# Performance work log

Hardware: AMD Instinct MI355X
Metric: run time of the kernel (lower is better)

The kernel has to match this reference:

```python
import jax, jax.numpy as jnp
import numpy as np
from jax import lax

EPS = 1e-5
DN = ('NCHW', 'OIHW', 'NCHW')


def binarize(x):
    # sign(x) with 0 -> +1, matching _STESign.forward
    return jnp.where(x >= 0, jnp.ones_like(x), -jnp.ones_like(x))


def batchnorm(x, g, b, m, v):
    # inference BatchNorm2d with running stats
    scale = (g / jnp.sqrt(v + EPS))[None, :, None, None]
    shift = (b - m * g / jnp.sqrt(v + EPS))[None, :, None, None]
    return x * scale + shift


def conv(x, w, stride):
    return lax.conv_general_dilated(x, w, (stride, stride), [(1, 1), (1, 1)],
                                    dimension_numbers=DN)


def setup_inputs() -> dict:
    key = jax.random.key(0)
    ks = jax.random.split(key, 24)
    d = {}
    d['x'] = jax.random.normal(ks[0], (32, 3, 224, 224), dtype=jnp.float32)
    d['conv1_w'] = jax.random.normal(ks[1], (32, 3, 3, 3), dtype=jnp.float32) * 0.1
    d['conv2_w'] = jax.random.normal(ks[2], (64, 32, 3, 3), dtype=jnp.float32) * 0.1
    d['conv3_w'] = jax.random.normal(ks[3], (128, 64, 3, 3), dtype=jnp.float32) * 0.1
    d['conv4_w'] = jax.random.normal(ks[4], (256, 128, 3, 3), dtype=jnp.float32) * 0.1
    for i, c in zip(range(1, 5), (32, 64, 128, 256)):
        base = 4 + (i - 1) * 4
        d[f'bn{i}_g'] = jax.random.uniform(ks[base + 1], (c,), dtype=jnp.float32) + 0.5
        d[f'bn{i}_b'] = jax.random.normal(ks[base + 2], (c,), dtype=jnp.float32) * 0.1
        d[f'bn{i}_m'] = jax.random.normal(ks[base + 3], (c,), dtype=jnp.float32) * 0.1
        d[f'bn{i}_v'] = jax.random.uniform(ks[base + 4], (c,), dtype=jnp.float32) + 0.5
    d['fc_w'] = jax.random.normal(ks[21], (2, 256), dtype=jnp.float32) * 0.05
    d['fc_b'] = jnp.zeros((2,), dtype=jnp.float32)
    return d


def reference(x, conv1_w, conv2_w, conv3_w, conv4_w,
              bn1_g, bn1_b, bn1_m, bn1_v,
              bn2_g, bn2_b, bn2_m, bn2_v,
              bn3_g, bn3_b, bn3_m, bn3_v,
              bn4_g, bn4_b, bn4_m, bn4_v,
              fc_w, fc_b):
    # conv1 (real) + bn1
    h = batchnorm(conv(x, conv1_w, 1), bn1_g, bn1_b, bn1_m, bn1_v)
    # BinarizeConv2d: binarize input and weight, then real conv
    h = binarize(batchnorm(conv(binarize(h), binarize(conv2_w), 2), bn2_g, bn2_b, bn2_m, bn2_v))
    h = binarize(batchnorm(conv(binarize(h), binarize(conv3_w), 2), bn3_g, bn3_b, bn3_m, bn3_v))
    h = binarize(batchnorm(conv(binarize(h), binarize(conv4_w), 2), bn4_g, bn4_b, bn4_m, bn4_v))
    # adaptive avg pool to 1x1 -> mean over H,W
    h = jnp.mean(h, axis=(2, 3))  # [B, 256]
    return h @ fc_w.T + fc_b
```

## Files before the change

### kernel.cpp

```cpp
#include <hip/hip_runtime.h>
#include <stdint.h>
#include <math.h>

#define OFF_T2     3712
#define OFF_T3     4224
#define OFF_T4     5248
#define OFF_W2     7296
#define OFF_W3     9600
#define OFF_W4     18816
#define OFF_A1     55680
#define OFF_A2     6478208
#define OFF_A3     9689472
#define OFF_CNT    11295104

#define C2_LW 116
#define C3_LW 58

static __device__ __forceinline__ float2 bnf(float g, float b, float m, float v) {
    float sc = __fdiv_rn(g, __fsqrt_rn(__fadd_rn(v, 1e-5f)));
    float sh = __fsub_rn(b, __fmul_rn(m, sc));
    return make_float2(sc, sh);
}
static __device__ __forceinline__ bool bnpos(float s, float2 p) {
    return __fadd_rn(__fmul_rn(s, p.x), p.y) >= 0.0f;
}
static __device__ __forceinline__ int find_T(int K, float2 p) {
    int lo = -K - 2, hi = K + 2;
    while (lo + 2 < hi) {
        int mid = ((lo + hi) >> 1) & ~1;
        if (bnpos((float)mid, p)) hi = mid; else lo = mid;
    }
    return hi;
}

#define CONV1_BLOCKS 3136
#define PREP_BLOCKS  1586

__global__ __launch_bounds__(256) void k_front(
    const float* __restrict__ x, const float* __restrict__ w1,
    const float* __restrict__ g1, const float* __restrict__ b1,
    const float* __restrict__ m1, const float* __restrict__ v1,
    const float* __restrict__ w2, const float* __restrict__ w3, const float* __restrict__ w4,
    const float* g2, const float* b2, const float* m2, const float* v2,
    const float* g3, const float* b3, const float* m3, const float* v3,
    const float* g4, const float* b4, const float* m4, const float* v4,
    uint32_t* __restrict__ A1,
    int* __restrict__ T2, int* __restrict__ T3, int* __restrict__ T4,
    uint32_t* __restrict__ W2, uint64_t* __restrict__ W3, uint64_t* __restrict__ W4)
{
    int tid = threadIdx.x;
    if (blockIdx.x >= CONV1_BLOCKS) {
        int gtid = (blockIdx.x - CONV1_BLOCKS) * 256 + tid;
        int wid  = gtid >> 6;
        int lane = gtid & 63;
        if (wid < 576) {
            int oc = wid / 9, t = wid - oc * 9;
            float v = (lane < 32) ? w2[oc * 288 + lane * 9 + t] : -1.0f;
            uint64_t m = __ballot(v >= 0.0f);
            if (lane == 0) W2[wid] = (uint32_t)m;
        } else if (wid < 1728) {
            int i = wid - 576;
            int oc = i / 9, t = i - oc * 9;
            float v = w3[oc * 576 + lane * 9 + t];
            uint64_t m = __ballot(v >= 0.0f);
            if (lane == 0) W3[i] = m;
        } else if (wid < 6336) {
            int i = wid - 1728;
            int oc = i / 18, rem = i - oc * 18;
            int t = rem >> 1, h = rem & 1;
            float v = w4[oc * 1152 + (h * 64 + lane) * 9 + t];
            uint64_t m = __ballot(v >= 0.0f);
            if (lane == 0) W4[i] = m;
        } else {
            int c = (wid - 6336) * 64 + lane;
            if (c < 64) {
                T2[c] = find_T(288, bnf(g2[c], b2[c], m2[c], v2[c]));
            } else if (c < 192) {
                int cc = c - 64;
                T3[cc] = find_T(576, bnf(g3[cc], b3[cc], m3[cc], v3[cc]));
            } else if (c < 448) {
                int cc = c - 192;
                T4[cc] = find_T(1152, bnf(g4[cc], b4[cc], m4[cc], v4[cc]));
            }
        }
        return;
    }

    __shared__ float  wl[27 * 32];
    __shared__ float2 s1[32];
    for (int i = tid; i < 864; i += 256) {
        int k = i >> 5, oc = i & 31;
        wl[i] = w1[oc * 27 + k];
    }
    if (tid < 32) s1[tid] = bnf(g1[tid], b1[tid], m1[tid], v1[tid]);
    __syncthreads();

    int idx = blockIdx.x * 256 + tid;
    int xp = idx % 112;
    int t  = idx / 112;
    int y  = t % 224;
    int b  = t / 224;
    int xc = xp * 2;

    const float* xb = x + (size_t)b * 150528;
    float xin[3][3][4];
    if ((unsigned)(y - 1) < 222u && (unsigned)(xp - 1) < 110u) {
        #pragma unroll
        for (int ic = 0; ic < 3; ic++)
            #pragma unroll
            for (int ky = 0; ky < 3; ky++) {
                const float* rp = xb + ic * 50176 + (y - 1 + ky) * 224 + (xc - 1);
                #pragma unroll
                for (int cx = 0; cx < 4; cx++) xin[ic][ky][cx] = rp[cx];
            }
    } else {
        #pragma unroll
        for (int ic = 0; ic < 3; ic++)
            #pragma unroll
            for (int ky = 0; ky < 3; ky++)
                #pragma unroll
                for (int cx = 0; cx < 4; cx++) {
                    int iy = y - 1 + ky, ix = xc - 1 + cx;
                    float v = 0.0f;
                    if ((unsigned)iy < 224u && (unsigned)ix < 224u)
                        v = xb[ic * 50176 + iy * 224 + ix];
                    xin[ic][ky][cx] = v;
                }
    }

    float acc0[32], acc1[32];
    #pragma unroll
    for (int oc = 0; oc < 32; oc++) { acc0[oc] = 0.0f; acc1[oc] = 0.0f; }

    const float4* wl4 = (const float4*)wl;
    #pragma unroll
    for (int k = 0; k < 27; k++) {
        int ic = k / 9, r = (k % 9) / 3, c = k % 3;
        float a0 = xin[ic][r][c];
        float a1 = xin[ic][r][c + 1];
        #pragma unroll
        for (int g8 = 0; g8 < 8; g8++) {
            float4 w = wl4[k * 8 + g8];
            acc0[g8*4+0] = fmaf(a0, w.x, acc0[g8*4+0]);
            acc0[g8*4+1] = fmaf(a0, w.y, acc0[g8*4+1]);
            acc0[g8*4+2] = fmaf(a0, w.z, acc0[g8*4+2]);
            acc0[g8*4+3] = fmaf(a0, w.w, acc0[g8*4+3]);
            acc1[g8*4+0] = fmaf(a1, w.x, acc1[g8*4+0]);
            acc1[g8*4+1] = fmaf(a1, w.y, acc1[g8*4+1]);
            acc1[g8*4+2] = fmaf(a1, w.z, acc1[g8*4+2]);
            acc1[g8*4+3] = fmaf(a1, w.w, acc1[g8*4+3]);
        }
    }

    uint32_t bits0 = 0, bits1 = 0;
    #pragma unroll
    for (int oc = 0; oc < 32; oc++) {
        float2 p = s1[oc];
        bits0 |= (uint32_t)bnpos(acc0[oc], p) << oc;
        bits1 |= (uint32_t)bnpos(acc1[oc], p) << oc;
    }
    uint2* dst = (uint2*)(A1 + (size_t)b * 50176 + y * 224 + xc);
    *dst = make_uint2(bits0, bits1);
}

template<unsigned VM>
static __device__ __forceinline__ bool pred2(const uint32_t (&w)[3][9], int j,
                                             const uint32_t (&wr)[9], int T) {
    int pc = 0;
    #pragma unroll
    for (int ky = 0; ky < 3; ky++)
        #pragma unroll
        for (int kx = 0; kx < 3; kx++) {
            int ti = ky * 3 + kx;
            if (VM & (1u << ti)) pc += __popc(w[ky][2 * j + kx] ^ wr[ti]);
        }
    constexpr int nv = __builtin_popcount(VM);
    return pc <= ((32 * nv - T) >> 1);
}

template<unsigned VM0, unsigned VM>
static __device__ __forceinline__ void group2(const uint32_t* lrow, int g,
        const uint32_t (&wr)[9], int T, uint64_t* dst, int lane) {
    uint32_t win[3][9];
    int c0 = 8 * g;
    #pragma unroll
    for (int r = 0; r < 3; r++) {
        const uint32_t* rp = lrow + r * C2_LW + c0;
        uint4 a = *(const uint4*)(rp);
        uint4 b = *(const uint4*)(rp + 4);
        win[r][0] = a.x; win[r][1] = a.y; win[r][2] = a.z; win[r][3] = a.w;
        win[r][4] = b.x; win[r][5] = b.y; win[r][6] = b.z; win[r][7] = b.w;
        win[r][8] = rp[8];
    }
    uint64_t b0 = __ballot(pred2<VM0>(win, 0, wr, T));
    uint64_t b1 = __ballot(pred2<VM >(win, 1, wr, T));
    uint64_t b2 = __ballot(pred2<VM >(win, 2, wr, T));
    uint64_t b3 = __ballot(pred2<VM >(win, 3, wr, T));
    if (lane == 0) {
        ulonglong2* d = (ulonglong2*)(dst + 4 * g);
        d[0] = make_ulonglong2(b0, b1);
        d[1] = make_ulonglong2(b2, b3);
    }
}

__global__ __launch_bounds__(256) void k_conv2(
    const uint32_t* __restrict__ A1, const uint32_t* __restrict__ W2g,
    const int* __restrict__ T2, uint64_t* __restrict__ A2)
{
    __shared__ __align__(16) uint32_t lds[9 * C2_LW];
    int bi = blockIdx.x;
    int b = bi / 56, rem = bi % 56;
    int oyq = rem >> 1, h = rem & 1;
    int xs = h * 56;
    int tid = threadIdx.x;
    const uint32_t* ap = A1 + (size_t)b * 50176;
    for (int i = tid; i < 9 * C2_LW; i += 256) {
        int r = i / C2_LW, c = i - r * C2_LW;
        int iy = oyq * 8 - 1 + r, ix = 2 * xs - 1 + c;
        uint32_t v = 0;
        if ((unsigned)iy < 224u && (unsigned)ix < 224u) v = ap[iy * 224 + ix];
        lds[i] = v;
    }
    __syncthreads();

    int w = tid >> 6, lane = tid & 63;
    int oy = oyq * 4 + w;
    uint32_t wr[9];
    #pragma unroll
    for (int ti = 0; ti < 9; ti++) wr[ti] = W2g[lane * 9 + ti];
    int T = T2[lane];
    const uint32_t* lrow = lds + 2 * w * C2_LW;
    uint64_t* dst = A2 + (size_t)b * 12544 + oy * 112 + xs;
    bool left = (xs == 0);

    if (oy == 0) {
        if (left) group2<0x1B0, 0x1F8>(lrow, 0, wr, T, dst, lane);
        else      group2<0x1F8, 0x1F8>(lrow, 0, wr, T, dst, lane);
        for (int g = 1; g < 14; g++) group2<0x1F8, 0x1F8>(lrow, g, wr, T, dst, lane);
    } else {
        if (left) group2<0x1B6, 0x1FF>(lrow, 0, wr, T, dst, lane);
        else      group2<0x1FF, 0x1FF>(lrow, 0, wr, T, dst, lane);
        for (int g = 1; g < 14; g++) group2<0x1FF, 0x1FF>(lrow, g, wr, T, dst, lane);
    }
}

template<unsigned VM>
static __device__ __forceinline__ bool pred3(const uint64_t (&w)[3][9], int j,
                                             const uint64_t (&wr)[9], int T) {
    int pc = 0;
    #pragma unroll
    for (int ky = 0; ky < 3; ky++)
        #pragma unroll
        for (int kx = 0; kx < 3; kx++) {
            int ti = ky * 3 + kx;
            if (VM & (1u << ti)) pc += __popcll(w[ky][2 * j + kx] ^ wr[ti]);
        }
    constexpr int nv = __builtin_popcount(VM);
    return pc <= ((64 * nv - T) >> 1);
}

template<unsigned VM0, unsigned VM>
static __device__ __forceinline__ void group3(const uint64_t* lrow, int g,
        const uint64_t (&wr)[9], int T, uint64_t* dst, int lane) {
    uint64_t win[3][9];
    int c0 = 8 * g;
    #pragma unroll
    for (int r = 0; r < 3; r++) {
        const uint64_t* rp = lrow + r * C3_LW + c0;
        ulonglong2 a0 = *(const ulonglong2*)(rp);
        ulonglong2 a1 = *(const ulonglong2*)(rp + 2);
        ulonglong2 a2 = *(const ulonglong2*)(rp + 4);
        ulonglong2 a3 = *(const ulonglong2*)(rp + 6);
        win[r][0] = a0.x; win[r][1] = a0.y; win[r][2] = a1.x; win[r][3] = a1.y;
        win[r][4] = a2.x; win[r][5] = a2.y; win[r][6] = a3.x; win[r][7] = a3.y;
        win[r][8] = rp[8];
    }
    uint64_t b0 = __ballot(pred3<VM0>(win, 0, wr, T));
    uint64_t b1 = __ballot(pred3<VM >(win, 1, wr, T));
    uint64_t b2 = __ballot(pred3<VM >(win, 2, wr, T));
    uint64_t b3 = __ballot(pred3<VM >(win, 3, wr, T));
    if (lane == 0) {
        ulonglong2* d = (ulonglong2*)(dst + 4 * g);
        d[0] = make_ulonglong2(b0, b1);
        d[1] = make_ulonglong2(b2, b3);
    }
}

__global__ __launch_bounds__(256) void k_conv3(
    const uint64_t* __restrict__ A2, const uint64_t* __restrict__ W3g,
    const int* __restrict__ T3, uint64_t* __restrict__ A3)
{
    __shared__ __align__(16) uint64_t lds[5 * C3_LW];
    int bi = blockIdx.x;
    int b = bi / 56, rem = bi % 56;
    int oyp = rem >> 1, h = rem & 1;
    int xs = h * 28;
    int tid = threadIdx.x;
    const uint64_t* ap = A2 + (size_t)b * 12544;
    for (int i = tid; i < 5 * C3_LW; i += 256) {
        int r = i / C3_LW, c = i - r * C3_LW;
        int iy = oyp * 4 - 1 + r, ix = 2 * xs - 1 + c;
        uint64_t v = 0;
        if ((unsigned)iy < 112u && (unsigned)ix < 112u) v = ap[iy * 112 + ix];
        lds[i] = v;
    }
    __syncthreads();

    int w = tid >> 6, lane = tid & 63;
    int oy = oyp * 2 + (w >> 1);
    int g  = w & 1;
    int oc = g * 64 + lane;
    uint64_t wr[9];
    #pragma unroll
    for (int ti = 0; ti < 9; ti++) wr[ti] = W3g[oc * 9 + ti];
    int T = T3[oc];
    const uint64_t* lrow = lds + 2 * (w >> 1) * C3_LW;
    uint64_t* dst = A3 + (size_t)g * 100352 + (size_t)b * 3136 + oy * 56 + xs;
    bool left = (xs == 0);

    if (oy == 0) {
        if (left) group3<0x1B0, 0x1F8>(lrow, 0, wr, T, dst, lane);
        else      group3<0x1F8, 0x1F8>(lrow, 0, wr, T, dst, lane);
        for (int gg = 1; gg < 7; gg++) group3<0x1F8, 0x1F8>(lrow, gg, wr, T, dst, lane);
    } else {
        if (left) group3<0x1B6, 0x1FF>(lrow, 0, wr, T, dst, lane);
        else      group3<0x1FF, 0x1FF>(lrow, 0, wr, T, dst, lane);
        for (int gg = 1; gg < 7; gg++) group3<0x1FF, 0x1FF>(lrow, gg, wr, T, dst, lane);
    }
}

template<unsigned VM>
static __device__ __forceinline__ bool pred4(const uint64_t (&w0)[3][5],
                                             const uint64_t (&w1)[3][5], int j,
                                             const ulonglong2 (&wr)[9], int T) {
    int pc = 0;
    #pragma unroll
    for (int ky = 0; ky < 3; ky++)
        #pragma unroll
        for (int kx = 0; kx < 3; kx++) {
            int ti = ky * 3 + kx;
            if (VM & (1u << ti)) {
                pc += __popcll(w0[ky][2 * j + kx] ^ wr[ti].x);
                pc += __popcll(w1[ky][2 * j + kx] ^ wr[ti].y);
            }
        }
    constexpr int nv = __builtin_popcount(VM);
    return pc <= ((128 * nv - T) >> 1);
}

template<unsigned VM0, unsigned VM>
static __device__ __forceinline__ int group4c(const uint64_t* ldsb, int g,
        const ulonglong2 (&wr)[9], int T) {
    uint64_t w0[3][5], w1[3][5];
    int c0 = 4 * g;
    #pragma unroll
    for (int r = 0; r < 3; r++) {
        const uint64_t* rp0 = ldsb + r * 30 + c0;
        const uint64_t* rp1 = ldsb + (3 + r) * 30 + c0;
        ulonglong2 a0 = *(const ulonglong2*)(rp0);
        ulonglong2 a1 = *(const ulonglong2*)(rp0 + 2);
        w0[r][0] = a0.x; w0[r][1] = a0.y; w0[r][2] = a1.x; w0[r][3] = a1.y;
        w0[r][4] = rp0[4];
        ulonglong2 b0 = *(const ulonglong2*)(rp1);
        ulonglong2 b1 = *(const ulonglong2*)(rp1 + 2);
        w1[r][0] = b0.x; w1[r][1] = b0.y; w1[r][2] = b1.x; w1[r][3] = b1.y;
        w1[r][4] = rp1[4];
    }
    int c = 0;
    c += pred4<VM0>(w0, w1, 0, wr, T) ? 1 : 0;
    c += pred4<VM >(w0, w1, 1, wr, T) ? 1 : 0;
    return c;
}

__global__ __launch_bounds__(256) void k_conv4(
    const uint64_t* __restrict__ A3, const uint64_t* __restrict__ W4g,
    const int* __restrict__ T4, int* __restrict__ CNT)
{
    __shared__ __align__(16) uint64_t lds[2 * 3 * 30];
    int bi = blockIdx.x;
    int b = bi / 56, rem = bi % 56;
    int oy = rem >> 1, h = rem & 1;
    int tid = threadIdx.x;
    const uint64_t* ap = A3 + (size_t)b * 3136;
    for (int i = tid; i < 174; i += 256) {
        int p = i / 87, j = i - p * 87;
        int r = j / 29, c = j - r * 29;
        int iy = 2 * oy - 1 + r, ix = 2 * h * 14 - 1 + c;
        uint64_t v = 0;
        if ((unsigned)iy < 56u && (unsigned)ix < 56u)
            v = ap[(size_t)p * 100352 + iy * 56 + ix];
        lds[(p * 3 + r) * 30 + c] = v;
    }
    __syncthreads();

    int w = tid >> 6, lane = tid & 63;
    int oc = w * 64 + lane;
    ulonglong2 wr[9];
    const ulonglong2* wp = (const ulonglong2*)(W4g + oc * 18);
    #pragma unroll
    for (int ti = 0; ti < 9; ti++) wr[ti] = wp[ti];
    int T = T4[oc];
    bool left = (h == 0);

    int cnt = 0;
    if (oy == 0) {
        if (left) cnt += group4c<0x1B0, 0x1F8>(lds, 0, wr, T);
        else      cnt += group4c<0x1F8, 0x1F8>(lds, 0, wr, T);
        for (int g = 1; g < 7; g++) cnt += group4c<0x1F8, 0x1F8>(lds, g, wr, T);
    } else {
        if (left) cnt += group4c<0x1B6, 0x1FF>(lds, 0, wr, T);
        else      cnt += group4c<0x1FF, 0x1FF>(lds, 0, wr, T);
        for (int g = 1; g < 7; g++) cnt += group4c<0x1FF, 0x1FF>(lds, g, wr, T);
    }
    atomicAdd(&CNT[b * 256 + oc], cnt);
}

__global__ __launch_bounds__(256) void k_tail(
    const int* __restrict__ CNT, const float* __restrict__ fcw,
    const float* __restrict__ fcb, float* __restrict__ out)
{
    int b = blockIdx.x;
    int c = threadIdx.x;
    int cnt = CNT[b * 256 + c];
    double mean = (2.0 * (double)cnt - 784.0) * (1.0 / 784.0);

    __shared__ double r0[256], r1[256];
    r0[c] = (double)fcw[c]       * mean;
    r1[c] = (double)fcw[256 + c] * mean;
    __syncthreads();
    for (int s = 128; s > 0; s >>= 1) {
        if (c < s) { r0[c] += r0[c + s]; r1[c] += r1[c + s]; }
        __syncthreads();
    }
    if (c == 0) {
        out[b * 2 + 0] = (float)(r0[0] + (double)fcb[0]);
        out[b * 2 + 1] = (float)(r1[0] + (double)fcb[1]);
    }
}

extern "C" void kernel_launch(void* const* d_in, const int* in_sizes, int n_in,
                              void* d_out, int out_size, void* d_ws, size_t ws_size,
                              hipStream_t stream) {
    const float* x   = (const float*)d_in[0];
    const float* w1  = (const float*)d_in[1];
    const float* w2  = (const float*)d_in[2];
    const float* w3  = (const float*)d_in[3];
    const float* w4  = (const float*)d_in[4];
    const float* g1 = (const float*)d_in[5],  *b1 = (const float*)d_in[6],
               * m1 = (const float*)d_in[7],  *v1 = (const float*)d_in[8];
    const float* g2 = (const float*)d_in[9],  *b2 = (const float*)d_in[10],
               * m2 = (const float*)d_in[11], *v2 = (const float*)d_in[12];
    const float* g3 = (const float*)d_in[13], *b3 = (const float*)d_in[14],
               * m3 = (const float*)d_in[15], *v3 = (const float*)d_in[16];
    const float* g4 = (const float*)d_in[17], *b4 = (const float*)d_in[18],
               * m4 = (const float*)d_in[19], *v4 = (const float*)d_in[20];
    const float* fcw = (const float*)d_in[21];
    const float* fcb = (const float*)d_in[22];
    float* out = (float*)d_out;

    char* ws = (char*)d_ws;
    int*      T2  = (int*)(ws + OFF_T2);
    int*      T3  = (int*)(ws + OFF_T3);
    int*      T4  = (int*)(ws + OFF_T4);
    uint32_t* W2  = (uint32_t*)(ws + OFF_W2);
    uint64_t* W3  = (uint64_t*)(ws + OFF_W3);
    uint64_t* W4  = (uint64_t*)(ws + OFF_W4);
    uint32_t* A1  = (uint32_t*)(ws + OFF_A1);
    uint64_t* A2  = (uint64_t*)(ws + OFF_A2);
    uint64_t* A3  = (uint64_t*)(ws + OFF_A3);
    int*      CNT = (int*)(ws + OFF_CNT);

    hipMemsetAsync(CNT, 0, 32 * 256 * sizeof(int), stream);
    hipLaunchKernelGGL(k_front, dim3(CONV1_BLOCKS + PREP_BLOCKS), dim3(256), 0, stream,
                       x, w1, g1, b1, m1, v1, w2, w3, w4,
                       g2, b2, m2, v2, g3, b3, m3, v3, g4, b4, m4, v4,
                       A1, T2, T3, T4, W2, W3, W4);
    hipLaunchKernelGGL(k_conv2, dim3(1792), dim3(256), 0, stream, A1, W2, T2, A2);
    hipLaunchKernelGGL(k_conv3, dim3(1792), dim3(256), 0, stream, A2, W3, T3, A3);
    hipLaunchKernelGGL(k_conv4, dim3(1792), dim3(256), 0, stream, A3, W4, T4, CNT);
    hipLaunchKernelGGL(k_tail,  dim3(32),   dim3(256), 0, stream, CNT, fcw, fcb, out);
}
```

Measured before the change: 217.6 us.

## Compute four pixels per thread in conv1 and fold CNT zeroing into front kernel

```diff
diff --git a/kernel.cpp b/kernel.cpp
--- a/kernel.cpp
+++ b/kernel.cpp
@@ -14,7 +14,6 @@
 #define OFF_CNT    11295104
 
 #define C2_LW 116
-#define C3_LW 58
 
 static __device__ __forceinline__ float2 bnf(float g, float b, float m, float v) {
     float sc = __fdiv_rn(g, __fsqrt_rn(__fadd_rn(v, 1e-5f)));
@@ -33,8 +32,8 @@
     return hi;
 }
 
-#define CONV1_BLOCKS 3136
-#define PREP_BLOCKS  1586
+#define CONV1_BLOCKS 1568
+#define PREP_BLOCKS  1618
 
 __global__ __launch_bounds__(256) void k_front(
     const float* __restrict__ x, const float* __restrict__ w1,
@@ -46,7 +45,8 @@
     const float* g4, const float* b4, const float* m4, const float* v4,
     uint32_t* __restrict__ A1,
     int* __restrict__ T2, int* __restrict__ T3, int* __restrict__ T4,
-    uint32_t* __restrict__ W2, uint64_t* __restrict__ W3, uint64_t* __restrict__ W4)
+    uint32_t* __restrict__ W2, uint64_t* __restrict__ W3, uint64_t* __restrict__ W4,
+    int* __restrict__ Z )
 {
     int tid = threadIdx.x;
     if (blockIdx.x >= CONV1_BLOCKS) {
@@ -71,7 +71,7 @@
             float v = w4[oc * 1152 + (h * 64 + lane) * 9 + t];
             uint64_t m = __ballot(v >= 0.0f);
             if (lane == 0) W4[i] = m;
-        } else {
+        } else if (wid < 6344) {
             int c = (wid - 6336) * 64 + lane;
             if (c < 64) {
                 T2[c] = find_T(288, bnf(g2[c], b2[c], m2[c], v2[c]));
@@ -82,6 +82,9 @@
                 int cc = c - 192;
                 T4[cc] = find_T(1152, bnf(g4[cc], b4[cc], m4[cc], v4[cc]));
             }
+        } else {
+            int zi = gtid - 406016;
+            if (zi < 8192) Z[zi] = 0;
         }
         return;
     }
@@ -95,72 +98,74 @@
     if (tid < 32) s1[tid] = bnf(g1[tid], b1[tid], m1[tid], v1[tid]);
     __syncthreads();
 
-    int idx = blockIdx.x * 256 + tid;
-    int xp = idx % 112;
-    int t  = idx / 112;
+    int q  = blockIdx.x * 256 + tid;
+    int xq = q % 56;
+    int t  = q / 56;
     int y  = t % 224;
     int b  = t / 224;
-    int xc = xp * 2;
+    int xc = xq * 4;
 
     const float* xb = x + (size_t)b * 150528;
-    float xin[3][3][4];
-    if ((unsigned)(y - 1) < 222u && (unsigned)(xp - 1) < 110u) {
-        #pragma unroll
-        for (int ic = 0; ic < 3; ic++)
+    bool interior = ((unsigned)(y - 1) < 222u) && ((unsigned)(xq - 1) < 54u);
+
+    float xin[9][6];
+    #pragma unroll
+    for (int ic = 0; ic < 3; ic++)
+        #pragma unroll
+        for (int ky = 0; ky < 3; ky++) {
+            int iy = y - 1 + ky;
+            const float* rp = xb + ic * 50176 + iy * 224 + (xc - 1);
+            float* xr = xin[ic * 3 + ky];
+            if (interior) {
+                #pragma unroll
+                for (int c = 0; c < 6; c++) xr[c] = rp[c];
+            } else {
+                #pragma unroll
+                for (int c = 0; c < 6; c++) {
+                    int ix = xc - 1 + c;
+                    xr[c] = ((unsigned)iy < 224u && (unsigned)ix < 224u) ? rp[c] : 0.0f;
+                }
+            }
+        }
+
+    const float4* wl4 = (const float4*)wl;
+    uint32_t bits0 = 0, bits1 = 0, bits2 = 0, bits3 = 0;
+
+    #pragma unroll 1
+    for (int og = 0; og < 8; og++) {
+        float acc[4][4];
+        #pragma unroll
+        for (int px = 0; px < 4; px++)
             #pragma unroll
-            for (int ky = 0; ky < 3; ky++) {
-                const float* rp = xb + ic * 50176 + (y - 1 + ky) * 224 + (xc - 1);
-                #pragma unroll
-                for (int cx = 0; cx < 4; cx++) xin[ic][ky][cx] = rp[cx];
+            for (int j = 0; j < 4; j++) acc[px][j] = 0.0f;
+
+        #pragma unroll
+        for (int k = 0; k < 27; k++) {
+            float4 w = wl4[k * 8 + og];
+            int row = k / 3, kx = k % 3;
+            #pragma unroll
+            for (int px = 0; px < 4; px++) {
+                float a = xin[row][kx + px];
+                acc[px][0] = fmaf(a, w.x, acc[px][0]);
+                acc[px][1] = fmaf(a, w.y, acc[px][1]);
+                acc[px][2] = fmaf(a, w.z, acc[px][2]);
+                acc[px][3] = fmaf(a, w.w, acc[px][3]);
             }
-    } else {
-        #pragma unroll
-        for (int ic = 0; ic < 3; ic++)
-            #pragma unroll
-            for (int ky = 0; ky < 3; ky++)
-                #pragma unroll
-                for (int cx = 0; cx < 4; cx++) {
-                    int iy = y - 1 + ky, ix = xc - 1 + cx;
-                    float v = 0.0f;
-                    if ((unsigned)iy < 224u && (unsigned)ix < 224u)
-                        v = xb[ic * 50176 + iy * 224 + ix];
-                    xin[ic][ky][cx] = v;
-                }
-    }
-
-    float acc0[32], acc1[32];
-    #pragma unroll
-    for (int oc = 0; oc < 32; oc++) { acc0[oc] = 0.0f; acc1[oc] = 0.0f; }
-
-    const float4* wl4 = (const float4*)wl;
-    #pragma unroll
-    for (int k = 0; k < 27; k++) {
-        int ic = k / 9, r = (k % 9) / 3, c = k % 3;
-        float a0 = xin[ic][r][c];
-        float a1 = xin[ic][r][c + 1];
-        #pragma unroll
-        for (int g8 = 0; g8 < 8; g8++) {
-            float4 w = wl4[k * 8 + g8];
-            acc0[g8*4+0] = fmaf(a0, w.x, acc0[g8*4+0]);
-            acc0[g8*4+1] = fmaf(a0, w.y, acc0[g8*4+1]);
-            acc0[g8*4+2] = fmaf(a0, w.z, acc0[g8*4+2]);
-            acc0[g8*4+3] = fmaf(a0, w.w, acc0[g8*4+3]);
-            acc1[g8*4+0] = fmaf(a1, w.x, acc1[g8*4+0]);
-            acc1[g8*4+1] = fmaf(a1, w.y, acc1[g8*4+1]);
-            acc1[g8*4+2] = fmaf(a1, w.z, acc1[g8*4+2]);
-            acc1[g8*4+3] = fmaf(a1, w.w, acc1[g8*4+3]);
-        }
-    }
-
-    uint32_t bits0 = 0, bits1 = 0;
-    #pragma unroll
-    for (int oc = 0; oc < 32; oc++) {
-        float2 p = s1[oc];
-        bits0 |= (uint32_t)bnpos(acc0[oc], p) << oc;
-        bits1 |= (uint32_t)bnpos(acc1[oc], p) << oc;
-    }
-    uint2* dst = (uint2*)(A1 + (size_t)b * 50176 + y * 224 + xc);
-    *dst = make_uint2(bits0, bits1);
+        }
+
+        #pragma unroll
+        for (int j = 0; j < 4; j++) {
+            float2 p = s1[og * 4 + j];
+            int sh = og * 4 + j;
+            bits0 |= (uint32_t)bnpos(acc[0][j], p) << sh;
+            bits1 |= (uint32_t)bnpos(acc[1][j], p) << sh;
+            bits2 |= (uint32_t)bnpos(acc[2][j], p) << sh;
+            bits3 |= (uint32_t)bnpos(acc[3][j], p) << sh;
+        }
+    }
+
+    uint4* dst = (uint4*)(A1 + (size_t)b * 50176 + y * 224 + xc);
+    *dst = make_uint4(bits0, bits1, bits2, bits3);
 }
 
 template<unsigned VM>
@@ -244,6 +249,7 @@
     }
 }
 
+#define C3_LW 58
 template<unsigned VM>
 static __device__ __forceinline__ bool pred3(const uint64_t (&w)[3][9], int j,
                                              const uint64_t (&wr)[9], int T) {
@@ -470,11 +476,10 @@
     uint64_t* A3  = (uint64_t*)(ws + OFF_A3);
     int*      CNT = (int*)(ws + OFF_CNT);
 
-    hipMemsetAsync(CNT, 0, 32 * 256 * sizeof(int), stream);
     hipLaunchKernelGGL(k_front, dim3(CONV1_BLOCKS + PREP_BLOCKS), dim3(256), 0, stream,
                        x, w1, g1, b1, m1, v1, w2, w3, w4,
                        g2, b2, m2, v2, g3, b3, m3, v3, g4, b4, m4, v4,
-                       A1, T2, T3, T4, W2, W3, W4);
+                       A1, T2, T3, T4, W2, W3, W4, CNT);
     hipLaunchKernelGGL(k_conv2, dim3(1792), dim3(256), 0, stream, A1, W2, T2, A2);
     hipLaunchKernelGGL(k_conv3, dim3(1792), dim3(256), 0, stream, A2, W3, T3, A3);
     hipLaunchKernelGGL(k_conv4, dim3(1792), dim3(256), 0, stream, A3, W4, T4, CNT);
```

New measurement: 215.6 us, median of 2. No clear change (-1.0%).
